# Performance work log

Hardware: AMD Instinct MI355X
Metric: run time of the kernel (lower is better)

Reference implementation:

```python
import jax, jax.numpy as jnp
import numpy as np

B, N, E, H, D, FF, L = 64, 200, 128, 8, 16, 512, 6
S = N + 1  # depot + nodes
EPS = 1e-5


def setup_inputs() -> dict:
    key = jax.random.key(0)
    ks = jax.random.split(key, 24)
    r = jax.random.normal
    HD = H * D
    inp = {
        "depot_xy": jax.random.uniform(ks[0], (B, 1, 3), dtype=jnp.float32),
        "node_xy_demand_tw": jax.random.uniform(ks[1], (B, N, 4), dtype=jnp.float32),
        "route_attn": r(ks[2], (B, H, S, S), dtype=jnp.float32),
        # initial embeddings
        "Wd": r(ks[3], (3, E)) * 0.3, "bd": jnp.zeros((E,)),
        "Wn": r(ks[4], (4, E)) * 0.3, "bn": jnp.zeros((E,)),
        # per-layer stacked params (leading dim L)
        "Wq": r(ks[5], (L, E, HD)) / np.sqrt(E),
        "Wk": r(ks[6], (L, E, HD)) / np.sqrt(E),
        "Wv": r(ks[7], (L, E, HD)) / np.sqrt(E),
        "Wo": r(ks[8], (L, HD, E)) / np.sqrt(HD), "bo": jnp.zeros((L, E)),
        # score_aggr MLP: in=head_num*aspect_num=2H, hidden=2H, out=H
        "A1w": r(ks[9], (L, 2 * H, 2 * H)) / np.sqrt(2 * H), "A1b": jnp.zeros((L, 2 * H)),
        "A2w": r(ks[10], (L, 2 * H, H)) / np.sqrt(2 * H), "A2b": jnp.zeros((L, H)),
        # instance-norm affine params
        "n1w": jnp.ones((L, E)), "n1b": jnp.zeros((L, E)),
        "n2w": jnp.ones((L, E)), "n2b": jnp.zeros((L, E)),
        # feed-forward
        "F1w": r(ks[11], (L, E, FF)) / np.sqrt(E), "F1b": jnp.zeros((L, FF)),
        "F2w": r(ks[12], (L, FF, E)) / np.sqrt(FF), "F2b": jnp.zeros((L, E)),
    }
    return inp


def _inorm(y, w, b):
    # InstanceNorm1d over the sequence axis (per batch, per channel), biased var, eps=1e-5
    m = jnp.mean(y, axis=1, keepdims=True)
    v = jnp.var(y, axis=1, keepdims=True)
    return (y - m) / jnp.sqrt(v + EPS) * w + b


def _encoder(depot_xy, node_xy_demand_tw, route_attn, Wd, bd, Wn, bn,
             Wq, Wk, Wv, Wo, bo, A1w, A1b, A2w, A2b,
             n1w, n1b, n2w, n2b, F1w, F1b, F2w, F2b):
    x = jnp.concatenate([depot_xy @ Wd + bd, node_xy_demand_tw @ Wn + bn], axis=1)  # [B,S,E]
    b, s = x.shape[0], x.shape[1]
    for l in range(L):
        heads = lambda t: t.reshape(b, s, H, D).transpose(0, 2, 1, 3)  # [B,H,S,D]
        q, k, v = heads(x @ Wq[l]), heads(x @ Wk[l]), heads(x @ Wv[l])
        score = jnp.einsum('bhnd,bhmd->bhnm', q, k)                    # [B,H,S,S]
        cat = jnp.concatenate([score, route_attn], axis=1)             # [B,2H,S,S]
        cat = cat.transpose(0, 2, 3, 1)                                # [B,S,S,2H]
        agg = jax.nn.relu(cat @ A1w[l] + A1b[l]) @ A2w[l] + A2b[l]     # [B,S,S,H]
        scaled = agg.transpose(0, 3, 1, 2)                             # [B,H,S,S]
        w = jax.nn.softmax(scaled, axis=-1)
        o = jnp.einsum('bhnm,bhmd->bhnd', w, v)                        # [B,H,S,D]
        o = o.transpose(0, 2, 1, 3).reshape(b, s, H * D)
        mh = o @ Wo[l] + bo[l]
        out1 = _inorm(x + mh, n1w[l], n1b[l])
        ff = jax.nn.relu(out1 @ F1w[l] + F1b[l]) @ F2w[l] + F2b[l]
        x = _inorm(out1 + ff, n2w[l], n2b[l])
    return x


def reference(depot_xy, node_xy_demand_tw, route_attn, Wd, bd, Wn, bn,
              Wq, Wk, Wv, Wo, bo, A1w, A1b, A2w, A2b,
              n1w, n1b, n2w, n2b, F1w, F1b, F2w, F2b):
    return _encoder(depot_xy, node_xy_demand_tw, route_attn, Wd, bd, Wn, bn,
                    Wq, Wk, Wv, Wo, bo, A1w, A1b, A2w, A2b,
                    n1w, n1b, n2w, n2b, F1w, F1b, F2w, F2b)
```

## Files before the change

kernel.cpp:

```cpp
#include <hip/hip_runtime.h>
#include <hip/hip_bf16.h>

#define B_   64
#define N_   200
#define S_   201
#define E_   128
#define H_   8
#define D_   16
#define HD_  128
#define FF_  512
#define L_   6
#define TWOH_ 16
#define NCH_  4
#define NCHB_ 51
#define PADM_ 208

typedef __hip_bfloat16 bf16;
typedef __attribute__((ext_vector_type(8))) short bfrag;
typedef __attribute__((ext_vector_type(4))) float f32x4;

__device__ __forceinline__ void split_bf16(float v, bf16& h, bf16& l) {
  h = __float2bfloat16(v);
  l = __float2bfloat16(v - __bfloat162float(h));
}

__global__ void embed_kernel(const float* __restrict__ depot, const float* __restrict__ node,
                             const float* __restrict__ Wd, const float* __restrict__ bd,
                             const float* __restrict__ Wn, const float* __restrict__ bn,
                             float* __restrict__ X, bf16* __restrict__ XBh, bf16* __restrict__ XBl) {
  int idx = blockIdx.x * blockDim.x + threadIdx.x;
  if (idx >= B_ * S_ * E_) return;
  int e  = idx & (E_ - 1);
  int bs = idx >> 7;
  int s  = bs % S_;
  int b  = bs / S_;
  float acc;
  if (s == 0) {
    acc = bd[e];
    #pragma unroll
    for (int i = 0; i < 3; ++i) acc += depot[b * 3 + i] * Wd[i * E_ + e];
  } else {
    acc = bn[e];
    const float* nd = node + ((size_t)b * N_ + (s - 1)) * 4;
    #pragma unroll
    for (int i = 0; i < 4; ++i) acc += nd[i] * Wn[i * E_ + e];
  }
  X[idx] = acc;
  bf16 hh, ll;
  split_bf16(acc, hh, ll);
  XBh[idx] = hh;
  XBl[idx] = ll;
}

__global__ void wcvt_kernel(const float* __restrict__ Wo, const float* __restrict__ F1w,
                            const float* __restrict__ F2w, const float* __restrict__ Wq,
                            const float* __restrict__ Wk, const float* __restrict__ Wv,
                            bf16* __restrict__ WTh, bf16* __restrict__ WTl) {
  int idx = blockIdx.x * blockDim.x + threadIdx.x;
  if (idx >= 1179648) return;
  float v;
  if (idx < 98304) {
    int l = idx / 16384, rr = idx % 16384;
    int e = rr / 128, h = rr % 128;
    v = Wo[(size_t)l * 16384 + h * 128 + e];
  } else if (idx < 491520) {
    int rem = idx - 98304;
    int l = rem / 65536, rr = rem % 65536;
    int f = rr / 128, e = rr % 128;
    v = F1w[(size_t)l * 65536 + e * 512 + f];
  } else if (idx < 884736) {
    int rem = idx - 491520;
    int l = rem / 65536, rr = rem % 65536;
    int e = rr / 512, f = rr % 512;
    v = F2w[(size_t)l * 65536 + f * 128 + e];
  } else {
    const float* src = (idx < 983040) ? Wq : (idx < 1081344) ? Wk : Wv;
    int rem = idx - ((idx < 983040) ? 884736 : (idx < 1081344) ? 983040 : 1081344);
    int l = rem / 16384, rr = rem % 16384;
    int hd = rr / 128, e = rr % 128;
    v = src[(size_t)l * 16384 + e * 128 + hd];
  }
  bf16 h, l2;
  split_bf16(v, h, l2);
  WTh[idx] = h;
  WTl[idx] = l2;
}

template<int EPI>
__global__ __launch_bounds__(256) void mgemm_kernel(
    const bf16* __restrict__ Ah, const bf16* __restrict__ Al,
    const bf16* __restrict__ BTh, const bf16* __restrict__ BTl,
    const float* __restrict__ bias, const float* __restrict__ res,
    float* __restrict__ Cf, bf16* __restrict__ Cbh, bf16* __restrict__ Cbl,
    int K, int Ntot) {
  __shared__ __align__(16) bf16 Ash[64][72];
  __shared__ __align__(16) bf16 Asl[64][72];
  __shared__ __align__(16) bf16 Bsh[64][72];
  __shared__ __align__(16) bf16 Bsl[64][72];
  int tid = threadIdx.x;
  int m0 = blockIdx.x * 64, n0 = blockIdx.y * 64;
  int lane = tid & 63, wave = tid >> 6;
  int wr = wave >> 1, wc = wave & 1;
  int la = lane & 15, lb = lane >> 4;
  f32x4 acc[2][2] = {};
  for (int k0 = 0; k0 < K; k0 += 64) {
    #pragma unroll
    for (int p = 0; p < 2; ++p) {
      int ch = tid + p * 256;
      int r = ch >> 3, kc = (ch & 7) << 3;
      size_t ga = (size_t)(m0 + r) * K + k0 + kc;
      size_t gb = (size_t)(n0 + r) * K + k0 + kc;
      *reinterpret_cast<bfrag*>(&Ash[r][kc]) = *reinterpret_cast<const bfrag*>(&Ah[ga]);
      *reinterpret_cast<bfrag*>(&Asl[r][kc]) = *reinterpret_cast<const bfrag*>(&Al[ga]);
      *reinterpret_cast<bfrag*>(&Bsh[r][kc]) = *reinterpret_cast<const bfrag*>(&BTh[gb]);
      *reinterpret_cast<bfrag*>(&Bsl[r][kc]) = *reinterpret_cast<const bfrag*>(&BTl[gb]);
    }
    __syncthreads();
    #pragma unroll
    for (int ks = 0; ks < 64; ks += 32) {
      bfrag ah0 = *(const bfrag*)&Ash[wr * 32 + la][ks + lb * 8];
      bfrag ah1 = *(const bfrag*)&Ash[wr * 32 + 16 + la][ks + lb * 8];
      bfrag al0 = *(const bfrag*)&Asl[wr * 32 + la][ks + lb * 8];
      bfrag al1 = *(const bfrag*)&Asl[wr * 32 + 16 + la][ks + lb * 8];
      bfrag bh0 = *(const bfrag*)&Bsh[wc * 32 + la][ks + lb * 8];
      bfrag bh1 = *(const bfrag*)&Bsh[wc * 32 + 16 + la][ks + lb * 8];
      bfrag bl0 = *(const bfrag*)&Bsl[wc * 32 + la][ks + lb * 8];
      bfrag bl1 = *(const bfrag*)&Bsl[wc * 32 + 16 + la][ks + lb * 8];
      acc[0][0] = __builtin_amdgcn_mfma_f32_16x16x32_bf16(ah0, bh0, acc[0][0], 0, 0, 0);
      acc[0][0] = __builtin_amdgcn_mfma_f32_16x16x32_bf16(ah0, bl0, acc[0][0], 0, 0, 0);
      acc[0][0] = __builtin_amdgcn_mfma_f32_16x16x32_bf16(al0, bh0, acc[0][0], 0, 0, 0);
      acc[0][1] = __builtin_amdgcn_mfma_f32_16x16x32_bf16(ah0, bh1, acc[0][1], 0, 0, 0);
      acc[0][1] = __builtin_amdgcn_mfma_f32_16x16x32_bf16(ah0, bl1, acc[0][1], 0, 0, 0);
      acc[0][1] = __builtin_amdgcn_mfma_f32_16x16x32_bf16(al0, bh1, acc[0][1], 0, 0, 0);
      acc[1][0] = __builtin_amdgcn_mfma_f32_16x16x32_bf16(ah1, bh0, acc[1][0], 0, 0, 0);
      acc[1][0] = __builtin_amdgcn_mfma_f32_16x16x32_bf16(ah1, bl0, acc[1][0], 0, 0, 0);
      acc[1][0] = __builtin_amdgcn_mfma_f32_16x16x32_bf16(al1, bh0, acc[1][0], 0, 0, 0);
      acc[1][1] = __builtin_amdgcn_mfma_f32_16x16x32_bf16(ah1, bh1, acc[1][1], 0, 0, 0);
      acc[1][1] = __builtin_amdgcn_mfma_f32_16x16x32_bf16(ah1, bl1, acc[1][1], 0, 0, 0);
      acc[1][1] = __builtin_amdgcn_mfma_f32_16x16x32_bf16(al1, bh1, acc[1][1], 0, 0, 0);
    }
    __syncthreads();
  }
  int r0 = lb * 4;
  #pragma unroll
  for (int ti = 0; ti < 2; ++ti)
    #pragma unroll
    for (int tj = 0; tj < 2; ++tj)
      #pragma unroll
      for (int j = 0; j < 4; ++j) {
        int m = m0 + wr * 32 + ti * 16 + r0 + j;
        int n = n0 + wc * 32 + tj * 16 + la;
        float v = acc[ti][tj][j];
        if (EPI == 1) {
          v += bias[n] + res[(size_t)m * Ntot + n];
          Cf[(size_t)m * Ntot + n] = v;
        } else if (EPI == 2) {
          v += bias[n];
          v = v > 0.f ? v : 0.f;
          bf16 vh, vl;
          split_bf16(v, vh, vl);
          Cbh[(size_t)m * Ntot + n] = vh;
          Cbl[(size_t)m * Ntot + n] = vl;
        } else {
          Cf[(size_t)m * Ntot + n] = v;
        }
      }
}

__global__ __launch_bounds__(256) void score_kernel(const float* __restrict__ Q,
                                                    const float* __restrict__ Kmat,
                                                    float* __restrict__ SC) {
  int bh = blockIdx.x;
  int h = bh & 7, b = bh >> 3;
  int nbase = blockIdx.y * 51;
  int ncnt = min(51, S_ - nbase);
  __shared__ __align__(16) float qs[51][20];
  __shared__ __align__(16) float ks[S_][20];
  int tid = threadIdx.x;
  for (int p = tid; p < 51 * 16; p += 256) {
    int r = p >> 4, d = p & 15;
    if (r < ncnt) qs[r][d] = Q[((size_t)(b * S_ + nbase + r)) * HD_ + h * D_ + d];
  }
  for (int p = tid; p < S_ * 16; p += 256) {
    int r = p >> 4, d = p & 15;
    ks[r][d] = Kmat[((size_t)(b * S_ + r)) * HD_ + h * D_ + d];
  }
  __syncthreads();
  float* out = SC + ((size_t)(b * H_ + h)) * S_ * S_;
  int tn = tid >> 4, tm = tid & 15;
  for (int n0 = tn * 2; n0 < ncnt; n0 += 32) {
    int n1v = (n0 + 1 < ncnt);
    f32x4 q0[4], q1[4];
    #pragma unroll
    for (int qd = 0; qd < 4; ++qd) {
      q0[qd] = *(const f32x4*)&qs[n0][qd * 4];
      q1[qd] = *(const f32x4*)&qs[n1v ? n0 + 1 : n0][qd * 4];
    }
    for (int m0 = tm * 2; m0 < S_; m0 += 32) {
      int m1v = (m0 + 1 < S_);
      float a00 = 0, a01 = 0, a10 = 0, a11 = 0;
      #pragma unroll
      for (int qd = 0; qd < 4; ++qd) {
        f32x4 k0 = *(const f32x4*)&ks[m0][qd * 4];
        f32x4 k1 = *(const f32x4*)&ks[m1v ? m0 + 1 : m0][qd * 4];
        #pragma unroll
        for (int c = 0; c < 4; ++c) {
          a00 += q0[qd][c] * k0[c];
          a01 += q0[qd][c] * k1[c];
          a10 += q1[qd][c] * k0[c];
          a11 += q1[qd][c] * k1[c];
        }
      }
      int gn = nbase + n0;
      out[(size_t)gn * S_ + m0] = a00;
      if (m1v) out[(size_t)gn * S_ + m0 + 1] = a01;
      if (n1v) {
        out[(size_t)(gn + 1) * S_ + m0] = a10;
        if (m1v) out[(size_t)(gn + 1) * S_ + m0 + 1] = a11;
      }
    }
  }
}

__global__ __launch_bounds__(256) void attn_kernel(
    const float* __restrict__ SC, const float* __restrict__ RA,
    const float* __restrict__ A1w, const float* __restrict__ A1b,
    const float* __restrict__ A2w, const float* __restrict__ A2b,
    const float* __restrict__ V, bf16* __restrict__ OBh, bf16* __restrict__ OBl) {
  int blk = blockIdx.x;
  int b  = blk / NCHB_;
  int n0 = (blk % NCHB_) * NCH_;
  int NV = min(NCH_, S_ - n0);
  __shared__ float PL[NCH_][H_][PADM_];
  __shared__ float partial[2][NCH_][H_][D_];
  __shared__ float inv[NCH_][H_];
  int tid = threadIdx.x;

  for (int e = tid; e < NV * S_; e += 256) {
    int nn = e / S_;
    int m  = e - nn * S_;
    const float* scp = SC + (((size_t)b * H_) * S_ + (n0 + nn)) * S_ + m;
    const float* rap = RA + (((size_t)b * H_) * S_ + (n0 + nn)) * S_ + m;
    float cc[TWOH_];
    #pragma unroll
    for (int h = 0; h < H_; ++h) {
      cc[h]      = scp[(size_t)h * S_ * S_];
      cc[H_ + h] = rap[(size_t)h * S_ * S_];
    }
    float h1[TWOH_];
    #pragma unroll
    for (int j = 0; j < TWOH_; ++j) h1[j] = A1b[j];
    #pragma unroll
    for (int i = 0; i < TWOH_; ++i) {
      float c = cc[i];
      #pragma unroll
      for (int j = 0; j < TWOH_; ++j)
        h1[j] += c * A1w[i * TWOH_ + j];
    }
    float agg[H_];
    #pragma unroll
    for (int h = 0; h < H_; ++h) agg[h] = A2b[h];
    #pragma unroll
    for (int j = 0; j < TWOH_; ++j) {
      float r = fmaxf(h1[j], 0.f);
      #pragma unroll
      for (int h = 0; h < H_; ++h)
        agg[h] += r * A2w[j * H_ + h];
    }
    #pragma unroll
    for (int h = 0; h < H_; ++h) PL[nn][h][m] = agg[h];
  }
  __syncthreads();

  {
    int g = tid >> 3, lane = tid & 7;
    int nn = g >> 3, h = g & 7;
    if (nn < NV) {
      float mx = -1e30f;
      for (int m = lane; m < S_; m += 8) mx = fmaxf(mx, PL[nn][h][m]);
      #pragma unroll
      for (int off = 4; off > 0; off >>= 1) mx = fmaxf(mx, __shfl_xor(mx, off, 8));
      float sum = 0.f;
      for (int m = lane; m < S_; m += 8) {
        float e = __expf(PL[nn][h][m] - mx);
        PL[nn][h][m] = e;
        sum += e;
      }
      #pragma unroll
      for (int off = 4; off > 0; off >>= 1) sum += __shfl_xor(sum, off, 8);
      if (lane == 0) inv[nn][h] = 1.f / sum;
    }
  }
  __syncthreads();

  {
    int half = tid >> 7, h = (tid >> 4) & 7, d = tid & 15;
    float a0 = 0.f, a1 = 0.f, a2 = 0.f, a3 = 0.f;
    const float* vp = V + (size_t)b * S_ * HD_ + h * D_ + d;
    for (int m = half; m < S_; m += 2) {
      float vv = vp[(size_t)m * HD_];
      a0 += PL[0][h][m] * vv;
      a1 += PL[1][h][m] * vv;
      a2 += PL[2][h][m] * vv;
      a3 += PL[3][h][m] * vv;
    }
    partial[half][0][h][d] = a0;
    partial[half][1][h][d] = a1;
    partial[half][2][h][d] = a2;
    partial[half][3][h][d] = a3;
  }
  __syncthreads();
  if (tid < 128) {
    int h = tid >> 4, d = tid & 15;
    #pragma unroll
    for (int nn = 0; nn < NCH_; ++nn)
      if (nn < NV) {
        float s = (partial[0][nn][h][d] + partial[1][nn][h][d]) * inv[nn][h];
        size_t o = ((size_t)b * S_ + (n0 + nn)) * HD_ + h * D_ + d;
        bf16 sh, sl;
        split_bf16(s, sh, sl);
        OBh[o] = sh;
        OBl[o] = sl;
      }
  }
}

__global__ __launch_bounds__(512) void inorm_kernel(const float* __restrict__ Y,
                                                    const float* __restrict__ w,
                                                    const float* __restrict__ bb,
                                                    float* __restrict__ X,
                                                    bf16* __restrict__ XBh,
                                                    bf16* __restrict__ XBl) {
  int b = blockIdx.x;
  int tid = threadIdx.x;
  int e = tid & 127, sg = tid >> 7;
  __shared__ float ps[4][128], pss[4][128];
  const float* base = Y + (size_t)b * S_ * E_;
  float s = 0.f, ss = 0.f;
  for (int i = sg; i < S_; i += 4) {
    float v = base[(size_t)i * E_ + e];
    s += v; ss += v * v;
  }
  ps[sg][e] = s; pss[sg][e] = ss;
  __syncthreads();
  if (sg == 0) {
    s  = ps[0][e] + ps[1][e] + ps[2][e] + ps[3][e];
    ss = pss[0][e] + pss[1][e] + pss[2][e] + pss[3][e];
    float mean = s / S_;
    float var  = fmaxf(ss / S_ - mean * mean, 0.f);
    float scale = rsqrtf(var + 1e-5f) * w[e];
    ps[0][e]  = scale;
    pss[0][e] = bb[e] - mean * scale;
  }
  __syncthreads();
  float scale = ps[0][e], shift = pss[0][e];
  float* dst = X + (size_t)b * S_ * E_;
  for (int i = sg; i < S_; i += 4) {
    size_t idx = (size_t)i * E_ + e;
    float v = base[idx] * scale + shift;
    dst[idx] = v;
    if (XBh) {
      size_t gi = (size_t)b * S_ * E_ + idx;
      bf16 vh, vl;
      split_bf16(v, vh, vl);
      XBh[gi] = vh;
      XBl[gi] = vl;
    }
  }
}

extern "C" void kernel_launch(void* const* d_in, const int* in_sizes, int n_in,
                              void* d_out, int out_size, void* d_ws, size_t ws_size,
                              hipStream_t stream) {
  const float* depot = (const float*)d_in[0];
  const float* node  = (const float*)d_in[1];
  const float* RA    = (const float*)d_in[2];
  const float* Wd    = (const float*)d_in[3];
  const float* bd    = (const float*)d_in[4];
  const float* Wn    = (const float*)d_in[5];
  const float* bn    = (const float*)d_in[6];
  const float* Wq    = (const float*)d_in[7];
  const float* Wk    = (const float*)d_in[8];
  const float* Wv    = (const float*)d_in[9];
  const float* Wo    = (const float*)d_in[10];
  const float* bo    = (const float*)d_in[11];
  const float* A1w   = (const float*)d_in[12];
  const float* A1b   = (const float*)d_in[13];
  const float* A2w   = (const float*)d_in[14];
  const float* A2b   = (const float*)d_in[15];
  const float* n1w   = (const float*)d_in[16];
  const float* n1b   = (const float*)d_in[17];
  const float* n2w   = (const float*)d_in[18];
  const float* n2b   = (const float*)d_in[19];
  const float* F1w   = (const float*)d_in[20];
  const float* F1b   = (const float*)d_in[21];
  const float* F2w   = (const float*)d_in[22];
  const float* F2b   = (const float*)d_in[23];

  const size_t XSZ  = (size_t)B_ * S_ * E_;
  const size_t SCSZ = (size_t)B_ * H_ * S_ * S_;
  const size_t XBF  = XSZ / 2;
  float* ws = (float*)d_ws;
  float* X   = ws;
  float* Q   = ws + XSZ;
  float* Kb  = ws + 2 * XSZ;
  float* V   = ws + 3 * XSZ;
  float* SC  = ws + 4 * XSZ;
  float* TMP = SC;
  bf16*  XBh = (bf16*)(SC + XSZ);
  bf16*  XBl = (bf16*)(SC + XSZ + XBF);
  bf16*  HBh = (bf16*)(SC + XSZ + 2 * XBF);
  bf16*  HBl = (bf16*)(SC + XSZ + 6 * XBF);
  float* tail = ws + 4 * XSZ + SCSZ;
  bf16*  WTh = (bf16*)tail;
  bf16*  WTl = (bf16*)(tail + 589824);
  bf16* OBh = (bf16*)Q;
  bf16* OBl = (bf16*)Kb;

  const int M = B_ * S_;

  wcvt_kernel<<<4608, 256, 0, stream>>>(Wo, F1w, F2w, Wq, Wk, Wv, WTh, WTl);
  embed_kernel<<<(B_ * S_ * E_ + 255) / 256, 256, 0, stream>>>(depot, node, Wd, bd, Wn, bn, X, XBh, XBl);

  for (int l = 0; l < L_; ++l) {
    mgemm_kernel<3><<<dim3(M / 64, 2), 256, 0, stream>>>(
        XBh, XBl, WTh + 884736 + (size_t)l * 16384, WTl + 884736 + (size_t)l * 16384,
        nullptr, nullptr, Q, nullptr, nullptr, E_, HD_);
    mgemm_kernel<3><<<dim3(M / 64, 2), 256, 0, stream>>>(
        XBh, XBl, WTh + 983040 + (size_t)l * 16384, WTl + 983040 + (size_t)l * 16384,
        nullptr, nullptr, Kb, nullptr, nullptr, E_, HD_);
    mgemm_kernel<3><<<dim3(M / 64, 2), 256, 0, stream>>>(
        XBh, XBl, WTh + 1081344 + (size_t)l * 16384, WTl + 1081344 + (size_t)l * 16384,
        nullptr, nullptr, V, nullptr, nullptr, E_, HD_);
    score_kernel<<<dim3(B_ * H_, 4), 256, 0, stream>>>(Q, Kb, SC);
    attn_kernel<<<B_ * NCHB_, 256, 0, stream>>>(SC, RA,
        A1w + (size_t)l * TWOH_ * TWOH_, A1b + (size_t)l * TWOH_,
        A2w + (size_t)l * TWOH_ * H_,    A2b + (size_t)l * H_, V, OBh, OBl);
    mgemm_kernel<1><<<dim3(M / 64, 2), 256, 0, stream>>>(
        OBh, OBl, WTh + (size_t)l * 16384, WTl + (size_t)l * 16384,
        bo + (size_t)l * E_, X, TMP, nullptr, nullptr, HD_, E_);
    inorm_kernel<<<B_, 512, 0, stream>>>(TMP, n1w + (size_t)l * E_, n1b + (size_t)l * E_, X, XBh, XBl);
    mgemm_kernel<2><<<dim3(M / 64, 8), 256, 0, stream>>>(
        XBh, XBl, WTh + 98304 + (size_t)l * 65536, WTl + 98304 + (size_t)l * 65536,
        F1b + (size_t)l * FF_, nullptr, nullptr, HBh, HBl, E_, FF_);
    mgemm_kernel<1><<<dim3(M / 64, 2), 256, 0, stream>>>(
        HBh, HBl, WTh + 491520 + (size_t)l * 65536, WTl + 491520 + (size_t)l * 65536,
        F2b + (size_t)l * E_, X, TMP, nullptr, nullptr, FF_, E_);
    float* dst = (l == L_ - 1) ? (float*)d_out : X;
    bf16* xh = (l == L_ - 1) ? nullptr : XBh;
    bf16* xl = (l == L_ - 1) ? nullptr : XBl;
    inorm_kernel<<<B_, 512, 0, stream>>>(TMP, n2w + (size_t)l * E_, n2b + (size_t)l * E_, dst, xh, xl);
  }
}
```

Before: 1.600 ms.

## Fuse Q and K projections into one GEMM and batch attn loads

Interleaves the Wq and Wk weights per layer so a single GEMM with N=256 writes a combined QK buffer, and the score kernel reads Q and K from it with a stride of 256. This removes one launch per layer. The attention kernel now issues all global loads for up to four elements per thread before doing the MLP math, to raise memory-level parallelism, at the cost of more registers. The PL shared-memory row padding is also changed to an odd stride to reduce bank conflicts.

```diff
diff --git a/kernel.cpp b/kernel.cpp
--- a/kernel.cpp
+++ b/kernel.cpp
@@ -13,7 +13,7 @@
 #define TWOH_ 16
 #define NCH_  4
 #define NCHB_ 51
-#define PADM_ 208
+#define PADM_ 209
 
 typedef __hip_bfloat16 bf16;
 typedef __attribute__((ext_vector_type(8))) short bfrag;
@@ -73,12 +73,18 @@
     int l = rem / 65536, rr = rem % 65536;
     int e = rr / 512, f = rr % 512;
     v = F2w[(size_t)l * 65536 + f * 128 + e];
+  } else if (idx < 1081344) {
+    int rem = idx - 884736;
+    int l = rem / 32768, rr = rem % 32768;
+    int n = rr / 128, e = rr % 128;
+    const float* src = (n < 128) ? Wq : Wk;
+    int hd = n & 127;
+    v = src[(size_t)l * 16384 + e * 128 + hd];
   } else {
-    const float* src = (idx < 983040) ? Wq : (idx < 1081344) ? Wk : Wv;
-    int rem = idx - ((idx < 983040) ? 884736 : (idx < 1081344) ? 983040 : 1081344);
+    int rem = idx - 1081344;
     int l = rem / 16384, rr = rem % 16384;
     int hd = rr / 128, e = rr % 128;
-    v = src[(size_t)l * 16384 + e * 128 + hd];
+    v = Wv[(size_t)l * 16384 + e * 128 + hd];
   }
   bf16 h, l2;
   split_bf16(v, h, l2);
@@ -167,8 +173,7 @@
       }
 }
 
-__global__ __launch_bounds__(256) void score_kernel(const float* __restrict__ Q,
-                                                    const float* __restrict__ Kmat,
+__global__ __launch_bounds__(256) void score_kernel(const float* __restrict__ QK,
                                                     float* __restrict__ SC) {
   int bh = blockIdx.x;
   int h = bh & 7, b = bh >> 3;
@@ -179,11 +184,11 @@
   int tid = threadIdx.x;
   for (int p = tid; p < 51 * 16; p += 256) {
     int r = p >> 4, d = p & 15;
-    if (r < ncnt) qs[r][d] = Q[((size_t)(b * S_ + nbase + r)) * HD_ + h * D_ + d];
+    if (r < ncnt) qs[r][d] = QK[((size_t)(b * S_ + nbase + r)) * 256 + h * D_ + d];
   }
   for (int p = tid; p < S_ * 16; p += 256) {
     int r = p >> 4, d = p & 15;
-    ks[r][d] = Kmat[((size_t)(b * S_ + r)) * HD_ + h * D_ + d];
+    ks[r][d] = QK[((size_t)(b * S_ + r)) * 256 + 128 + h * D_ + d];
   }
   __syncthreads();
   float* out = SC + ((size_t)(b * H_ + h)) * S_ * S_;
@@ -236,39 +241,52 @@
   __shared__ float inv[NCH_][H_];
   int tid = threadIdx.x;
 
-  for (int e = tid; e < NV * S_; e += 256) {
-    int nn = e / S_;
-    int m  = e - nn * S_;
-    const float* scp = SC + (((size_t)b * H_) * S_ + (n0 + nn)) * S_ + m;
-    const float* rap = RA + (((size_t)b * H_) * S_ + (n0 + nn)) * S_ + m;
-    float cc[TWOH_];
-    #pragma unroll
-    for (int h = 0; h < H_; ++h) {
-      cc[h]      = scp[(size_t)h * S_ * S_];
-      cc[H_ + h] = rap[(size_t)h * S_ * S_];
-    }
-    float h1[TWOH_];
-    #pragma unroll
-    for (int j = 0; j < TWOH_; ++j) h1[j] = A1b[j];
-    #pragma unroll
-    for (int i = 0; i < TWOH_; ++i) {
-      float c = cc[i];
-      #pragma unroll
-      for (int j = 0; j < TWOH_; ++j)
-        h1[j] += c * A1w[i * TWOH_ + j];
-    }
-    float agg[H_];
-    #pragma unroll
-    for (int h = 0; h < H_; ++h) agg[h] = A2b[h];
-    #pragma unroll
-    for (int j = 0; j < TWOH_; ++j) {
-      float r = fmaxf(h1[j], 0.f);
-      #pragma unroll
-      for (int h = 0; h < H_; ++h)
-        agg[h] += r * A2w[j * H_ + h];
-    }
-    #pragma unroll
-    for (int h = 0; h < H_; ++h) PL[nn][h][m] = agg[h];
+  {
+    float cc[4][TWOH_];
+    int   mm[4], nnv[4];
+    bool  val[4];
+    #pragma unroll
+    for (int s = 0; s < 4; ++s) {
+      int e = tid + s * 256;
+      val[s] = (e < NV * S_);
+      int nn = e / S_;
+      int m  = e - nn * S_;
+      if (!val[s]) { nn = 0; m = 0; }
+      nnv[s] = nn; mm[s] = m;
+      const float* scp = SC + (((size_t)b * H_) * S_ + (n0 + nn)) * S_ + m;
+      const float* rap = RA + (((size_t)b * H_) * S_ + (n0 + nn)) * S_ + m;
+      #pragma unroll
+      for (int h = 0; h < H_; ++h) {
+        cc[s][h]      = scp[(size_t)h * S_ * S_];
+        cc[s][H_ + h] = rap[(size_t)h * S_ * S_];
+      }
+    }
+    #pragma unroll
+    for (int s = 0; s < 4; ++s) {
+      if (!val[s]) continue;
+      float h1[TWOH_];
+      #pragma unroll
+      for (int j = 0; j < TWOH_; ++j) h1[j] = A1b[j];
+      #pragma unroll
+      for (int i = 0; i < TWOH_; ++i) {
+        float c = cc[s][i];
+        #pragma unroll
+        for (int j = 0; j < TWOH_; ++j)
+          h1[j] += c * A1w[i * TWOH_ + j];
+      }
+      float agg[H_];
+      #pragma unroll
+      for (int h = 0; h < H_; ++h) agg[h] = A2b[h];
+      #pragma unroll
+      for (int j = 0; j < TWOH_; ++j) {
+        float r = fmaxf(h1[j], 0.f);
+        #pragma unroll
+        for (int h = 0; h < H_; ++h)
+          agg[h] += r * A2w[j * H_ + h];
+      }
+      #pragma unroll
+      for (int h = 0; h < H_; ++h) PL[nnv[s]][h][mm[s]] = agg[h];
+    }
   }
   __syncthreads();
 
@@ -402,8 +420,7 @@
   const size_t XBF  = XSZ / 2;
   float* ws = (float*)d_ws;
   float* X   = ws;
-  float* Q   = ws + XSZ;
-  float* Kb  = ws + 2 * XSZ;
+  float* QK  = ws + XSZ;
   float* V   = ws + 3 * XSZ;
   float* SC  = ws + 4 * XSZ;
   float* TMP = SC;
@@ -414,8 +431,8 @@
   float* tail = ws + 4 * XSZ + SCSZ;
   bf16*  WTh = (bf16*)tail;
   bf16*  WTl = (bf16*)(tail + 589824);
-  bf16* OBh = (bf16*)Q;
-  bf16* OBl = (bf16*)Kb;
+  bf16* OBh = (bf16*)QK;
+  bf16* OBl = (bf16*)(ws + 2 * XSZ);
 
   const int M = B_ * S_;
 
@@ -423,16 +440,13 @@
   embed_kernel<<<(B_ * S_ * E_ + 255) / 256, 256, 0, stream>>>(depot, node, Wd, bd, Wn, bn, X, XBh, XBl);
 
   for (int l = 0; l < L_; ++l) {
-    mgemm_kernel<3><<<dim3(M / 64, 2), 256, 0, stream>>>(
-        XBh, XBl, WTh + 884736 + (size_t)l * 16384, WTl + 884736 + (size_t)l * 16384,
-        nullptr, nullptr, Q, nullptr, nullptr, E_, HD_);
-    mgemm_kernel<3><<<dim3(M / 64, 2), 256, 0, stream>>>(
-        XBh, XBl, WTh + 983040 + (size_t)l * 16384, WTl + 983040 + (size_t)l * 16384,
-        nullptr, nullptr, Kb, nullptr, nullptr, E_, HD_);
+    mgemm_kernel<3><<<dim3(M / 64, 4), 256, 0, stream>>>(
+        XBh, XBl, WTh + 884736 + (size_t)l * 32768, WTl + 884736 + (size_t)l * 32768,
+        nullptr, nullptr, QK, nullptr, nullptr, E_, 256);
     mgemm_kernel<3><<<dim3(M / 64, 2), 256, 0, stream>>>(
         XBh, XBl, WTh + 1081344 + (size_t)l * 16384, WTl + 1081344 + (size_t)l * 16384,
         nullptr, nullptr, V, nullptr, nullptr, E_, HD_);
-    score_kernel<<<dim3(B_ * H_, 4), 256, 0, stream>>>(Q, Kb, SC);
+    score_kernel<<<dim3(B_ * H_, 4), 256, 0, stream>>>(QK, SC);
     attn_kernel<<<B_ * NCHB_, 256, 0, stream>>>(SC, RA,
         A1w + (size_t)l * TWOH_ * TWOH_, A1b + (size_t)l * TWOH_,
         A2w + (size_t)l * TWOH_ * H_,    A2b + (size_t)l * H_, V, OBh, OBl);
```

Result: faster. 1.507 ms (-5.8%).
